# Optimization experiments

Measured on AMD Instinct MI355X. Metric: run time of the kernel, lower is better.

Reference implementation:

```python
import jax, jax.numpy as jnp
import numpy as np

H = 128; R = 8; VN = 100; VA = 64
N = 8192; B = 64; L = 48; E = 65536


def setup_inputs() -> dict:
    key = jax.random.key(0)
    ks = jax.random.split(key, 24)
    s = 0.05
    nodeTypes = jax.random.randint(ks[0], (N,), 0, VN)
    edge_index = jax.random.randint(ks[1], (2, E), 0, N)
    edge_attr = jax.random.randint(ks[2], (E,), 0, R)
    bs = jnp.repeat(jnp.arange(B), N // B)              # sorted node->graph map
    nodes_bs = jnp.full((B,), N // B, dtype=jnp.int32)  # nodes per graph
    len_seq = jax.random.randint(ks[3], (B,), 1, L + 1).at[0].set(L)  # max == L
    sequence_input = (jax.random.uniform(ks[4], (N, L)) < 0.05).astype(jnp.float32)
    action_input = jax.random.randint(ks[5], (B,), 0, VA)
    params = dict(
        emb_nodes=jax.random.normal(ks[6], (VN, H)) * s,
        emb_actions=jax.random.normal(ks[7], (VA, H)) * s,
        rgcn_rel=jax.random.normal(ks[8], (3, R, H, H)) * s,   # per-layer relation weights
        rgcn_root=jax.random.normal(ks[9], (3, H, H)) * s,
        rgcn_bias=jnp.zeros((3, H)),
        gru_w_ih=jax.random.normal(ks[10], (3 * H, H)) * s,
        gru_w_hh=jax.random.normal(ks[11], (3 * H, H)) * s,
        gru_b_ih=jnp.zeros((3 * H,)),
        gru_b_hh=jnp.zeros((3 * H,)),
        linA_w=jax.random.normal(ks[12], (H, H)) * s,
        linA_b=jnp.zeros((H,)),
        linAf_w=jax.random.normal(ks[13], (VA, H)) * s,
        linAf_b=jnp.zeros((VA,)),
        linN_w=jax.random.normal(ks[14], (H, 2 * H)) * s,
        linN_b=jnp.zeros((H,)),
        linNf_w=jax.random.normal(ks[15], (1, H)) * s,
        linNf_b=jnp.zeros((1,)),
    )
    return dict(nodeTypes=nodeTypes, edge_index=edge_index, edge_attr=edge_attr,
                bs=bs, nodes_bs=nodes_bs, len_seq=len_seq,
                sequence_input=sequence_input, action_input=action_input, **params)


def reference(nodeTypes, edge_index, edge_attr, bs, nodes_bs, len_seq,
              sequence_input, action_input,
              emb_nodes, emb_actions, rgcn_rel, rgcn_root, rgcn_bias,
              gru_w_ih, gru_w_hh, gru_b_ih, gru_b_hh,
              linA_w, linA_b, linAf_w, linAf_b,
              linN_w, linN_b, linNf_w, linNf_b):
    n = nodeTypes.shape[0]
    b = nodes_bs.shape[0]
    h = emb_nodes.shape[1]
    r = rgcn_rel.shape[1]
    l = sequence_input.shape[1]

    x = emb_nodes[nodeTypes]                               # [N,H]
    src, dst = edge_index[0], edge_index[1]
    seg = dst * r + edge_attr                              # per (target, relation) segment
    cnt = jax.ops.segment_sum(jnp.ones((src.shape[0],), x.dtype), seg, n * r)
    denom = jnp.maximum(cnt, 1.0).reshape(n, r, 1)
    for li in range(3):
        agg = jax.ops.segment_sum(x[src], seg, n * r).reshape(n, r, h) / denom
        x = jax.nn.relu(jnp.einsum('nrh,rho->no', agg, rgcn_rel[li])
                        + x @ rgcn_root[li] + rgcn_bias[li])

    # global mean pool -> graph embedding
    h_G = jax.ops.segment_sum(x, bs, b) / nodes_bs[:, None].astype(x.dtype)  # [B,H]
    action = jax.nn.relu(h_G @ linA_w.T + linA_b) @ linAf_w.T + linAf_b      # [B,VA]

    sos = emb_actions[action_input][:, None, :]            # [B,1,H]
    # sequence embeddings: sum over nodes in each graph of seq[i,t]*x[i]
    emb_seq = sequence_input[:, :, None] * x[:, None, :]   # [N,L,H]
    out = jax.ops.segment_sum(emb_seq, bs, b)              # [B,L,H]
    input_gru = jnp.concatenate([sos, out], axis=1)[:, :l] # packed GRU only sees first L steps

    # single-layer GRU, h0 = h_G (torch gate order r,z,n)
    xW = input_gru @ gru_w_ih.T + gru_b_ih                 # [B,L,3H]
    def step(hprev, xw):
        hW = hprev @ gru_w_hh.T + gru_b_hh
        xr, xz, xn = jnp.split(xw, 3, -1)
        hr, hz, hn = jnp.split(hW, 3, -1)
        rg = jax.nn.sigmoid(xr + hr)
        zg = jax.nn.sigmoid(xz + hz)
        ng = jnp.tanh(xn + rg * hn)
        hnew = (1.0 - zg) * ng + zg * hprev
        return hnew, hnew
    _, hs = jax.lax.scan(step, h_G, jnp.swapaxes(xW, 0, 1))
    seq_out = jnp.swapaxes(hs, 0, 1)                       # [B,L,H]
    mask = jnp.arange(l)[None, :] < len_seq[:, None]       # pad_packed zero-pads
    seq_out = seq_out * mask[:, :, None]

    out_gru = seq_out[bs]                                  # repeat_interleave -> [N,L,H]
    concats = jnp.concatenate(
        [out_gru, jnp.broadcast_to(x[:, None, :], (n, l, h))], axis=2)  # [N,L,2H]
    hid = jax.nn.relu(concats @ linN_w.T + linN_b)         # [N,L,H]
    logits = (hid @ linNf_w.T + linNf_b)[..., 0]           # [N,L]

    # scatter_softmax over nodes grouped by graph (dim 0)
    m = jax.lax.stop_gradient(jax.ops.segment_max(logits, bs, b))
    e = jnp.exp(logits - m[bs])
    ssum = jax.ops.segment_sum(e, bs, b)
    nodes_final = e / ssum[bs]
    return action, nodes_final
```

## Files before the change

### kernel.cpp

```cpp
#include <hip/hip_runtime.h>
#include <hip/hip_bf16.h>

#define H   128
#define RR  8
#define NN  8192
#define BB  64
#define LL  48
#define EE  65536
#define NPG 128
#define VA  64
#define NSEG (NN*RR)
#define GPB 16

typedef unsigned short u16;
typedef unsigned int   u32;

__device__ __forceinline__ float b2f(u16 u) {
    union { u32 i; float f; } v; v.i = ((u32)u) << 16; return v.f;
}
__device__ __forceinline__ u16 f2b(float f) {
    union { float f; u32 i; } v; v.f = f;
    u32 x = v.i;
    return (u16)((x + 0x7fffu + ((x >> 16) & 1u)) >> 16);
}
__device__ __forceinline__ float2 up2(u32 p) {
    union { u32 i; float f; } a, b;
    a.i = p << 16; b.i = p & 0xffff0000u;
    return make_float2(a.f, b.f);
}
__device__ __forceinline__ u32 pk2(float a, float b) {
    return ((u32)f2b(b) << 16) | (u32)f2b(a);
}
__device__ __forceinline__ float rcpf(float x) { return __builtin_amdgcn_rcpf(x); }
__device__ __forceinline__ u32 cvtpk(float lo, float hi) {
    u32 r;
    asm("v_cvt_pk_bf16_f32 %0, %1, %2" : "=v"(r) : "v"(lo), "v"(hi));
    return r;
}

#define K_LOG2E  1.4426950408889634f
#define K_2LOG2E 2.8853900817779268f

typedef __attribute__((ext_vector_type(8))) short bf16x8;
typedef __attribute__((ext_vector_type(4))) float f32x4;
typedef __attribute__((ext_vector_type(4))) unsigned short u16x4;

__global__ __launch_bounds__(256) void k_init(const int* __restrict__ nodeTypes,
                                              const float* __restrict__ emb_nodes,
                                              float* __restrict__ x0,
                                              int* __restrict__ fill) {
    int idx = blockIdx.x * 256 + threadIdx.x;
    if (idx < NSEG) fill[idx] = 0;
    if (idx < NN * H) {
        int n = idx >> 7, h = idx & (H - 1);
        x0[idx] = emb_nodes[(size_t)nodeTypes[n] * H + h];
    }
}

__global__ __launch_bounds__(256) void k_hist(const int* __restrict__ edge_index,
                                              const int* __restrict__ edge_attr,
                                              int* __restrict__ fill) {
    int e = blockIdx.x * 256 + threadIdx.x;
    if (e < EE) {
        int seg = edge_index[EE + e] * RR + edge_attr[e];
        atomicAdd(&fill[seg], 1);
    }
}

__global__ __launch_bounds__(256) void k_scan1(const int* __restrict__ fill,
                                               int* __restrict__ bsum) {
    __shared__ int red[4];
    int tid = threadIdx.x, lane = tid & 63, wv = tid >> 6;
    int v = fill[blockIdx.x * 256 + tid];
#pragma unroll
    for (int off = 32; off >= 1; off >>= 1) v += __shfl_down(v, off, 64);
    if (lane == 0) red[wv] = v;
    __syncthreads();
    if (tid == 0) bsum[blockIdx.x] = red[0] + red[1] + red[2] + red[3];
}

__global__ __launch_bounds__(256) void k_scan2(const int* __restrict__ bsum,
                                               int* __restrict__ boff,
                                               int* __restrict__ rowptr) {
    __shared__ int s[256];
    int tid = threadIdx.x;
    int v0 = bsum[tid];
    s[tid] = v0;
    __syncthreads();
    for (int off = 1; off < 256; off <<= 1) {
        int v = (tid >= off) ? s[tid - off] : 0;
        __syncthreads();
        s[tid] += v;
        __syncthreads();
    }
    boff[tid] = s[tid] - v0;
    if (tid == 255) rowptr[NSEG] = s[255];
}

__global__ __launch_bounds__(256) void k_scan3(const int* __restrict__ boff,
                                               int* __restrict__ fill,
                                               int* __restrict__ rowptr) {
    __shared__ int s[256];
    int tid = threadIdx.x;
    int g = blockIdx.x * 256 + tid;
    int c = fill[g];
    s[tid] = c;
    __syncthreads();
    for (int off = 1; off < 256; off <<= 1) {
        int v = (tid >= off) ? s[tid - off] : 0;
        __syncthreads();
        s[tid] += v;
        __syncthreads();
    }
    int r = boff[blockIdx.x] + s[tid] - c;
    rowptr[g] = r;
    fill[g] = r;
}

__global__ __launch_bounds__(256) void k_scatter(const int* __restrict__ edge_index,
                                                 const int* __restrict__ edge_attr,
                                                 int* __restrict__ fill,
                                                 int* __restrict__ colidx) {
    int e = blockIdx.x * 256 + threadIdx.x;
    if (e < EE) {
        int seg = edge_index[EE + e] * RR + edge_attr[e];
        int pos = atomicAdd(&fill[seg], 1);
        colidx[pos] = edge_index[e];
    }
}

__global__ __launch_bounds__(256) void k_wprep(const float* __restrict__ rel,
                                               const float* __restrict__ root,
                                               const float* __restrict__ w_ih,
                                               u16* __restrict__ WTt,
                                               u16* __restrict__ WTih,
                                               float* __restrict__ hGsum) {
    int idx = blockIdx.x * 256 + threadIdx.x;
    if (idx < 384 * H) WTih[idx] = f2b(w_ih[idx]);
    if (idx < BB * H) hGsum[idx] = 0.f;
    if (idx >= 3 * 147456) return;
    int li  = idx / 147456;
    int rem = idx - li * 147456;
    int tile = rem / 36864;
    int r2   = rem - tile * 36864;
    int ks   = r2 / 1024;
    int r3   = r2 - ks * 1024;
    int sub  = r3 >> 9;
    int r4   = r3 & 511;
    int lane = r4 >> 3, j = r4 & 7;
    int col = tile * 32 + sub * 16 + (lane & 15);
    int k   = ks * 32 + (lane >> 4) * 8 + j;
    float v;
    if (k < 1024) v = rel[(((size_t)li * RR + (k >> 7)) * H + (k & 127)) * H + col];
    else          v = root[((size_t)li * H + (k - 1024)) * H + col];
    WTt[idx] = f2b(v);
}

#define RGN 16
#define EPRE 512

__global__ __launch_bounds__(256) void k_rgcn(const float* __restrict__ xin,
                                              float* __restrict__ xout,
                                              const u16* __restrict__ WTt,
                                              const float* __restrict__ bias,
                                              const int* __restrict__ rowptr,
                                              const int* __restrict__ colidx,
                                              float* __restrict__ hGsum) {
    __shared__ u32 ab[RGN * 580];
    __shared__ int begs[RGN * RR + 1];
    __shared__ int eidx[EPRE];
    int tid = threadIdx.x, wv = tid >> 6, lane = tid & 63;
    int n0 = blockIdx.x * RGN, segbase = n0 * RR;

    if (tid <= RGN * RR) begs[tid] = rowptr[segbase + tid];
    __syncthreads();
    int E0 = begs[0], ne = begs[RGN * RR] - E0;
    for (int i = tid; i < ne && i < EPRE; i += 256) eidx[i] = colidx[E0 + i];
    __syncthreads();

    for (int s = wv; s < RGN * RR; s += 4) {
        int beg = begs[s], end = begs[s + 1];
        float a0 = 0.f, a1 = 0.f;
        for (int e = beg; e < end; ++e) {
            int off = e - E0;
            int src = (off < EPRE) ? eidx[off] : colidx[e];
            float2 v = ((const float2*)(xin + (size_t)src * H))[lane];
            a0 += v.x; a1 += v.y;
        }
        float inv = 1.f / fmaxf((float)(end - beg), 1.f);
        ab[(s >> 3) * 580 + ((s & 7) << 6) + lane] = pk2(a0 * inv, a1 * inv);
    }
    for (int i = wv; i < RGN; i += 4) {
        const float* xr = xin + (size_t)(n0 + i) * H + 2 * lane;
        ab[i * 580 + 512 + lane] = pk2(xr[0], xr[1]);
    }
    __syncthreads();

    int m = lane & 15, quad = lane >> 4;
    int colbase = wv * 32;
    const u32* aP = ab + m * 580 + quad * 4;
    const u32* bT = (const u32*)WTt + (size_t)wv * 36 * 512 + lane * 4;
    f32x4 acc0 = {0.f, 0.f, 0.f, 0.f}, acc1 = {0.f, 0.f, 0.f, 0.f};
    bf16x8 b0c = *(const bf16x8*)bT;
    bf16x8 b1c = *(const bf16x8*)(bT + 256);
    for (int ks = 0; ks < 36; ++ks) {
        bf16x8 b0n, b1n;
        if (ks < 35) {
            b0n = *(const bf16x8*)(bT + (ks + 1) * 512);
            b1n = *(const bf16x8*)(bT + (ks + 1) * 512 + 256);
        }
        bf16x8 a = *(const bf16x8*)(aP + ks * 16);
        acc0 = __builtin_amdgcn_mfma_f32_16x16x32_bf16(a, b0c, acc0, 0, 0, 0);
        acc1 = __builtin_amdgcn_mfma_f32_16x16x32_bf16(a, b1c, acc1, 0, 0, 0);
        b0c = b0n; b1c = b1n;
    }
    int c0 = colbase + m, c1 = c0 + 16;
    float bv0 = bias[c0], bv1 = bias[c1];
    float so0 = 0.f, so1 = 0.f;
#pragma unroll
    for (int rg = 0; rg < 4; ++rg) {
        int n = n0 + quad * 4 + rg;
        float o0 = fmaxf(acc0[rg] + bv0, 0.f);
        float o1 = fmaxf(acc1[rg] + bv1, 0.f);
        xout[(size_t)n * H + c0] = o0;
        xout[(size_t)n * H + c1] = o1;
        so0 += o0; so1 += o1;
    }
    if (hGsum) {
        so0 += __shfl_xor(so0, 16, 64);
        so0 += __shfl_xor(so0, 32, 64);
        so1 += __shfl_xor(so1, 16, 64);
        so1 += __shfl_xor(so1, 32, 64);
        if (quad == 0) {
            int g = n0 >> 7;
            atomicAdd(&hGsum[g * H + c0], so0);
            atomicAdd(&hGsum[g * H + c1], so1);
        }
    }
}

__global__ __launch_bounds__(128) void k_pool_act(const float* __restrict__ hGsum,
                                                  const int* __restrict__ nodes_bs,
                                                  const float* __restrict__ linA_w,
                                                  const float* __restrict__ linA_b,
                                                  const float* __restrict__ linAf_w,
                                                  const float* __restrict__ linAf_b,
                                                  float* __restrict__ hG,
                                                  float* __restrict__ out) {
    __shared__ float hgs[H], t1[H];
    int b = blockIdx.x, h = threadIdx.x;
    float hg = hGsum[(size_t)b * H + h] / (float)nodes_bs[b];
    hG[(size_t)b * H + h] = hg;
    hgs[h] = hg;
    __syncthreads();
    float acc = linA_b[h];
    const float* wr = linA_w + (size_t)h * H;
    for (int k = 0; k < H; ++k) acc += wr[k] * hgs[k];
    t1[h] = fmaxf(acc, 0.f);
    __syncthreads();
    if (h < VA) {
        float a = linAf_b[h];
        const float* w2 = linAf_w + (size_t)h * H;
        for (int k = 0; k < H; ++k) a += w2[k] * t1[k];
        out[(size_t)b * VA + h] = a;
    }
}

__global__ __launch_bounds__(256) void k_seqpool(const float* __restrict__ xf,
                                                 const float* __restrict__ seq,
                                                 const float* __restrict__ emb_actions,
                                                 const int* __restrict__ action_input,
                                                 float* __restrict__ igG) {
    __shared__ float xg[64][H];
    __shared__ u16 lists[LL][64];
    __shared__ int cnts[LL];
    int b = blockIdx.x, tid = threadIdx.x;
    int col = tid & 127, tg = tid >> 7;
    float acc[24];
#pragma unroll
    for (int m = 0; m < 24; ++m) acc[m] = 0.f;

    for (int chunk = 0; chunk < 2; ++chunk) {
        int i0 = b * NPG + chunk * 64;
        __syncthreads();
        if (tid < LL) cnts[tid] = 0;
        __syncthreads();
        for (int idx = tid; idx < 64 * H / 4; idx += 256)
            ((float4*)&xg[0][0])[idx] = ((const float4*)(xf + (size_t)i0 * H))[idx];
        for (int idx = tid; idx < 64 * LL; idx += 256) {
            int i = idx / LL, t = idx - i * LL;
            if (seq[(size_t)(i0 + i) * LL + t] != 0.f) {
                int p = atomicAdd(&cnts[t], 1);
                lists[t][p] = (u16)i;
            }
        }
        __syncthreads();
        for (int m = 0; m < 24; ++m) {
            int t = tg + 2 * m;
            int c = cnts[t];
            float a = acc[m];
            for (int p = 0; p < c; ++p) a += xg[lists[t][p]][col];
            acc[m] = a;
        }
    }
    if (tid < H)
        igG[((size_t)b * LL) * H + tid] = emb_actions[(size_t)action_input[b] * H + tid];
#pragma unroll
    for (int m = 0; m < 24; ++m) {
        int t = tg + 2 * m;
        if (t < LL - 1)
            igG[((size_t)b * LL + t + 1) * H + col] = acc[m];
    }
}

__global__ __launch_bounds__(256) void k_xw(const float* __restrict__ igG,
                                            const u16* __restrict__ WTih,
                                            const float* __restrict__ b_ih,
                                            const float* __restrict__ b_hh,
                                            u16* __restrict__ xwG) {
    __shared__ u32 ab[16 * 68];
    int tid = threadIdx.x, wv = tid >> 6, lane = tid & 63;
    int n0 = blockIdx.x * 16;
    for (int s = tid; s < 16 * 64; s += 256) {
        int row = s >> 6, kp = s & 63;
        float2 v = *(const float2*)(igG + (size_t)(n0 + row) * H + 2 * kp);
        ab[row * 68 + kp] = pk2(v.x, v.y);
    }
    __syncthreads();
    int m = lane & 15, quad = lane >> 4;
    const u32* aP = ab + m * 68 + quad * 4;
    f32x4 acc[6];
#pragma unroll
    for (int i = 0; i < 6; ++i) acc[i] = (f32x4){0.f, 0.f, 0.f, 0.f};
#pragma unroll
    for (int ks = 0; ks < 4; ++ks) {
        bf16x8 a = *(const bf16x8*)(aP + ks * 16);
#pragma unroll
        for (int tc = 0; tc < 6; ++tc) {
            int colr = wv * 96 + tc * 16 + m;
            bf16x8 bfr = *(const bf16x8*)((const u32*)WTih + (size_t)colr * 64 + quad * 4 + ks * 16);
            acc[tc] = __builtin_amdgcn_mfma_f32_16x16x32_bf16(a, bfr, acc[tc], 0, 0, 0);
        }
    }
#pragma unroll
    for (int tc = 0; tc < 6; ++tc) {
        int c = wv * 96 + tc * 16 + m;
        float bv = b_ih[c] + ((c < 256) ? b_hh[c] : 0.f);
        float sc = (c < 256) ? K_LOG2E : K_2LOG2E;
        int R = c & 127, gate = c >> 7;
#pragma unroll
        for (int rg = 0; rg < 4; ++rg) {
            int r = n0 + quad * 4 + rg;
            int bb = r / 48, tt = r - bb * 48;
            size_t o = (((((size_t)(bb >> 4) * LL + tt) * 8 + (R >> 4)) * 3 + gate) * 256)
                     + (((R >> 2) & 3) << 6) + ((bb & 15) << 2) + (R & 3);
            xwG[o] = f2b((acc[tc][rg] + bv) * sc);
        }
    }
}

__global__ __launch_bounds__(512) void k_gruM(const u16* __restrict__ xw2,
                                              const float* __restrict__ hG,
                                              const float* __restrict__ w_hh,
                                              const float* __restrict__ b_hh,
                                              const int* __restrict__ len_seq,
                                              float* __restrict__ soutG) {
    __shared__ __align__(16) u16 hA[2][2][2048];
    int tid = threadIdx.x;
    int lane = tid & 63, wv = tid >> 6;
    int mi = lane & 15, quad = lane >> 4;
    int gblk = blockIdx.x;
    int g_abs = gblk * GPB + mi;
    int R0 = 16 * wv + 4 * quad;

    int eW = (((wv >> 1) * 64) + (mi + 16 * ((2 * wv + (quad >> 1)) & 3))) * 8
             + 4 * (quad & 1);

    bf16x8 wfr[3][4];
#pragma unroll
    for (int gate = 0; gate < 3; ++gate) {
        int T = wv + 8 * gate;
        float sc = (gate == 2) ? K_2LOG2E : K_LOG2E;
#pragma unroll
        for (int ks = 0; ks < 4; ++ks) {
            const float* wp = w_hh + (size_t)(16 * T + mi) * H + quad * 8 + ks * 32;
            float4 f0 = *(const float4*)wp;
            float4 f1 = *(const float4*)(wp + 4);
            bf16x8 v;
            v[0] = (short)f2b(f0.x * sc); v[1] = (short)f2b(f0.y * sc);
            v[2] = (short)f2b(f0.z * sc); v[3] = (short)f2b(f0.w * sc);
            v[4] = (short)f2b(f1.x * sc); v[5] = (short)f2b(f1.y * sc);
            v[6] = (short)f2b(f1.z * sc); v[7] = (short)f2b(f1.w * sc);
            wfr[gate][ks] = v;
        }
    }
    float4 bn = *(const float4*)(b_hh + 256 + R0);
    float4 h0 = *(const float4*)(hG + (size_t)g_abs * H + R0);
    int ls = len_seq[g_abs];

    float hp[4]  = {h0.x, h0.y, h0.z, h0.w};
    float bnn[4] = {bn.x * K_2LOG2E, bn.y * K_2LOG2E, bn.z * K_2LOG2E, bn.w * K_2LOG2E};

    auto storeh = [&](int buf, const float* hv) {
        u32 w0 = cvtpk(hv[0], hv[1]);
        u32 w1 = cvtpk(hv[2], hv[3]);
        float2 e0 = up2(w0), e1 = up2(w1);
        u32 l0 = cvtpk(hv[0] - e0.x, hv[1] - e0.y);
        u32 l1 = cvtpk(hv[2] - e1.x, hv[3] - e1.y);
        *(uint2*)&hA[buf][0][eW] = make_uint2(w0, w1);
        *(uint2*)&hA[buf][1][eW] = make_uint2(l0, l1);
    };
    auto loadxw = [&](int t, u16x4* d) {
        const u16* p = xw2 + ((((size_t)gblk * LL + t) * 8 + wv) * 3) * 256
                     + (quad << 6) + (mi << 2);
        d[0] = *(const u16x4*)(p);
        d[1] = *(const u16x4*)(p + 256);
        d[2] = *(const u16x4*)(p + 512);
    };

    auto step = [&](int t, const u16x4* x, int buf) {
        f32x4 acc[3];
        acc[0] = (f32x4){0.f, 0.f, 0.f, 0.f};
        acc[1] = (f32x4){0.f, 0.f, 0.f, 0.f};
        acc[2] = (f32x4){bnn[0], bnn[1], bnn[2], bnn[3]};
#pragma unroll
        for (int ks = 0; ks < 4; ++ks) {
            const int e = (ks * 64 + lane) * 8;
            bf16x8 bh = *(const bf16x8*)&hA[buf][0][e];
            bf16x8 bl = *(const bf16x8*)&hA[buf][1][e];
#pragma unroll
            for (int gate = 0; gate < 3; ++gate) {
                acc[gate] = __builtin_amdgcn_mfma_f32_16x16x32_bf16(wfr[gate][ks], bh, acc[gate], 0, 0, 0);
                acc[gate] = __builtin_amdgcn_mfma_f32_16x16x32_bf16(wfr[gate][ks], bl, acc[gate], 0, 0, 0);
            }
        }
        float hv[4];
        float4 so;
#pragma unroll
        for (int r = 0; r < 4; ++r) {
            float xr = b2f(x[0][r]);
            float xz = b2f(x[1][r]);
            float xn = b2f(x[2][r]);
            float rg = rcpf(1.f + __builtin_amdgcn_exp2f(-(xr + acc[0][r])));
            float zg = rcpf(1.f + __builtin_amdgcn_exp2f(-(xz + acc[1][r])));
            float u  = xn + rg * acc[2][r];
            float ng = 1.f - 2.f * rcpf(__builtin_amdgcn_exp2f(u) + 1.f);
            float hn = ng + zg * (hp[r] - ng);
            hp[r] = hn;
            hv[r] = hn;
            ((float*)&so)[r] = (t < ls) ? hn : 0.f;
        }
        *(float4*)(soutG + ((size_t)g_abs * LL + t) * H + R0) = so;
        storeh(buf ^ 1, hv);
    };

    u16x4 xa[3], xb[3];
    loadxw(0, xa);
    loadxw(1, xb);
    storeh(0, hp);
    asm volatile("s_waitcnt lgkmcnt(0)\n\ts_barrier" ::: "memory");

    for (int t = 0; t < LL; t += 2) {
        step(t, xa, 0);
        if (t + 2 < LL) loadxw(t + 2, xa);
        asm volatile("s_waitcnt lgkmcnt(0)\n\ts_barrier" ::: "memory");
        step(t + 1, xb, 1);
        if (t + 3 < LL) loadxw(t + 3, xb);
        asm volatile("s_waitcnt lgkmcnt(0)\n\ts_barrier" ::: "memory");
    }
}

__global__ __launch_bounds__(256) void k_a2(const float* __restrict__ soutG,
                                            const float* __restrict__ linN_w,
                                            float* __restrict__ A2) {
    __shared__ float wb[32][130];
    __shared__ float xl[16][H];
    int tid = threadIdx.x;
    int n0 = blockIdx.x * 16;
    for (int idx = tid; idx < 16 * H; idx += 256)
        xl[idx >> 7][idx & 127] = soutG[(size_t)n0 * H + idx];
    int col = tid & 127, g = tid >> 7;
    float acc[8] = {0.f, 0.f, 0.f, 0.f, 0.f, 0.f, 0.f, 0.f};
    for (int c = 0; c < 4; ++c) {
        int k0 = c * 32;
        __syncthreads();
        for (int idx = tid; idx < 32 * H; idx += 256) {
            int r = idx >> 5, kk = idx & 31;
            wb[kk][r] = linN_w[(size_t)r * (2 * H) + k0 + kk];
        }
        __syncthreads();
#pragma unroll
        for (int kk = 0; kk < 32; ++kk) {
            float w = wb[kk][col];
#pragma unroll
            for (int j = 0; j < 8; ++j) acc[j] += xl[g * 8 + j][k0 + kk] * w;
        }
    }
#pragma unroll
    for (int j = 0; j < 8; ++j)
        A2[(size_t)(n0 + g * 8 + j) * H + col] = acc[j];
}

__global__ __launch_bounds__(256) void k_bx(const float* __restrict__ xf,
                                            const float* __restrict__ linN_w,
                                            const float* __restrict__ linN_b,
                                            u16* __restrict__ BxU) {
    __shared__ float wb[32][130];
    __shared__ float xl[16][H];
    int tid = threadIdx.x;
    int n0 = blockIdx.x * 16;
    for (int idx = tid; idx < 16 * H; idx += 256)
        xl[idx >> 7][idx & 127] = xf[(size_t)n0 * H + idx];
    int col = tid & 127, g = tid >> 7;
    float bv = linN_b[col];
    float acc[8] = {bv, bv, bv, bv, bv, bv, bv, bv};
    for (int c = 0; c < 4; ++c) {
        int k0 = c * 32;
        __syncthreads();
        for (int idx = tid; idx < 32 * H; idx += 256) {
            int r = idx >> 5, kk = idx & 31;
            wb[kk][r] = linN_w[(size_t)r * (2 * H) + H + k0 + kk];
        }
        __syncthreads();
#pragma unroll
        for (int kk = 0; kk < 32; ++kk) {
            float w = wb[kk][col];
#pragma unroll
            for (int j = 0; j < 8; ++j) acc[j] += xl[g * 8 + j][k0 + kk] * w;
        }
    }
#pragma unroll
    for (int j = 0; j < 8; ++j)
        BxU[(size_t)(n0 + g * 8 + j) * H + col] = f2b(acc[j]);
}

__global__ __launch_bounds__(256) void k_logits(const float* __restrict__ A2,
                                                const u16* __restrict__ BxU,
                                                const float* __restrict__ linNf_w,
                                                float* __restrict__ logits) {
    __shared__ float a2s[LL][130];
    __shared__ float bxs[16][130];
    __shared__ float w2s[H];
    int tid = threadIdx.x;
    int g = blockIdx.x >> 3, tile = blockIdx.x & 7;
    int n0g = g * NPG + tile * 16;

    for (int i2 = tid; i2 < LL * 64; i2 += 256) {
        int r = i2 >> 6, c2 = i2 & 63;
        *(float2*)&a2s[r][2 * c2] = *(const float2*)(A2 + ((size_t)g * LL + r) * H + 2 * c2);
    }
    for (int iu = tid; iu < 16 * 64; iu += 256) {
        int r = iu >> 6, c = iu & 63;
        float2 v = up2(((const u32*)BxU)[(size_t)(n0g + r) * 64 + c]);
        *(float2*)&bxs[r][2 * c] = v;
    }
    if (tid < H) w2s[tid] = linNf_w[tid];
    __syncthreads();

    int n = tid & 15, tt = tid >> 4;
#pragma unroll
    for (int pass = 0; pass < 3; ++pass) {
        int t = tt + 16 * pass;
        float acc = 0.f;
#pragma unroll
        for (int kp = 0; kp < 64; ++kp) {
            float2 a2 = *(const float2*)&a2s[t][2 * kp];
            float2 bx = *(const float2*)&bxs[n][2 * kp];
            float2 w  = *(const float2*)&w2s[2 * kp];
            acc += w.x * fmaxf(a2.x + bx.x, 0.f) + w.y * fmaxf(a2.y + bx.y, 0.f);
        }
        logits[(size_t)(n0g + n) * LL + t] = acc;
    }
}

__global__ __launch_bounds__(256) void k_softmax(const float* __restrict__ logits,
                                                 float* __restrict__ out) {
    __shared__ float lg[NPG][LL + 1];
    __shared__ float pm[4][LL], ps[4][LL];
    __shared__ float mv[LL], inv[LL];
    int b = blockIdx.x, tid = threadIdx.x;
    int n0 = b * NPG;
    for (int idx = tid; idx < NPG * LL; idx += 256) {
        int n = idx / LL, t = idx - n * LL;
        lg[n][t] = logits[(size_t)n0 * LL + idx];
    }
    __syncthreads();
    int t = tid & 63, seg = tid >> 6;
    if (t < LL) {
        float m = -1e30f;
        int nb = seg * 32;
        for (int n = nb; n < nb + 32; ++n) m = fmaxf(m, lg[n][t]);
        pm[seg][t] = m;
    }
    __syncthreads();
    if (tid < LL)
        mv[tid] = fmaxf(fmaxf(pm[0][tid], pm[1][tid]), fmaxf(pm[2][tid], pm[3][tid]));
    __syncthreads();
    if (t < LL) {
        float m = mv[t], s = 0.f;
        int nb = seg * 32;
        for (int n = nb; n < nb + 32; ++n) {
            float e = __expf(lg[n][t] - m);
            lg[n][t] = e;
            s += e;
        }
        ps[seg][t] = s;
    }
    __syncthreads();
    if (tid < LL)
        inv[tid] = 1.f / (ps[0][tid] + ps[1][tid] + ps[2][tid] + ps[3][tid]);
    __syncthreads();
    for (int idx = tid; idx < NPG * LL; idx += 256) {
        int n = idx / LL, tc = idx - n * LL;
        out[(size_t)BB * VA + (size_t)n0 * LL + idx] = lg[n][tc] * inv[tc];
    }
}

extern "C" void kernel_launch(void* const* d_in, const int* in_sizes, int n_in,
                              void* d_out, int out_size, void* d_ws, size_t ws_size,
                              hipStream_t stream) {
    (void)in_sizes; (void)n_in; (void)out_size; (void)ws_size;
    const int*   nodeTypes    = (const int*)d_in[0];
    const int*   edge_index   = (const int*)d_in[1];
    const int*   edge_attr    = (const int*)d_in[2];
    const int*   nodes_bs     = (const int*)d_in[4];
    const int*   len_seq      = (const int*)d_in[5];
    const float* seq_in       = (const float*)d_in[6];
    const int*   action_input = (const int*)d_in[7];
    const float* emb_nodes    = (const float*)d_in[8];
    const float* emb_actions  = (const float*)d_in[9];
    const float* rgcn_rel     = (const float*)d_in[10];
    const float* rgcn_root    = (const float*)d_in[11];
    const float* rgcn_bias    = (const float*)d_in[12];
    const float* gru_w_ih     = (const float*)d_in[13];
    const float* gru_w_hh     = (const float*)d_in[14];
    const float* gru_b_ih     = (const float*)d_in[15];
    const float* gru_b_hh     = (const float*)d_in[16];
    const float* linA_w       = (const float*)d_in[17];
    const float* linA_b       = (const float*)d_in[18];
    const float* linAf_w      = (const float*)d_in[19];
    const float* linAf_b      = (const float*)d_in[20];
    const float* linN_w       = (const float*)d_in[21];
    const float* linN_b       = (const float*)d_in[22];
    const float* linNf_w      = (const float*)d_in[23];

    char* w = (char*)d_ws;
    float* x0      = (float*)(w + 0);
    u16*   xwG     = (u16*)  (w + 0);
    float* logitsW = (float*)(w + 0);
    float* soutG   = (float*)(w + 2359296);
    float* x1      = (float*)(w + 4194304);
    float* igG     = (float*)(w + 8388608);
    float* A2      = (float*)(w + 8388608);
    u16*   BxU     = (u16*)  (w + 9961472);
    int*   bsum    = (int*)  (w + 9961472);
    int*   boff    = (int*)  (w + 9962496);
    float* hGsum   = (float*)(w + 9969664);
    int*   rowptr  = (int*)  (w + 11567104);
    int*   fill    = (int*)  (w + 11829760);
    u16*   WTih    = (u16*)  (w + 11829760);
    float* hG      = (float*)(w + 12058624);
    int*   colidx  = (int*)  (w + 12091904);
    u16*   WT      = (u16*)  (w + 12616192);

    float* out_f = (float*)d_out;

    k_init<<<dim3(4096), dim3(256), 0, stream>>>(nodeTypes, emb_nodes, x0, fill);
    k_hist<<<dim3(256), dim3(256), 0, stream>>>(edge_index, edge_attr, fill);
    k_scan1<<<dim3(256), dim3(256), 0, stream>>>(fill, bsum);
    k_scan2<<<dim3(1), dim3(256), 0, stream>>>(bsum, boff, rowptr);
    k_scan3<<<dim3(256), dim3(256), 0, stream>>>(boff, fill, rowptr);
    k_scatter<<<dim3(256), dim3(256), 0, stream>>>(edge_index, edge_attr, fill, colidx);
    k_wprep<<<dim3(1728), dim3(256), 0, stream>>>(rgcn_rel, rgcn_root, gru_w_ih,
                                                  WT, WTih, hGsum);

    const int rg_grid = NN / RGN;
    k_rgcn<<<dim3(rg_grid), dim3(256), 0, stream>>>(x0, x1,
        WT + 0 * 147456, rgcn_bias + 0 * H, rowptr, colidx, nullptr);
    k_rgcn<<<dim3(rg_grid), dim3(256), 0, stream>>>(x1, x0,
        WT + 1 * 147456, rgcn_bias + 1 * H, rowptr, colidx, nullptr);
    k_rgcn<<<dim3(rg_grid), dim3(256), 0, stream>>>(x0, x1,
        WT + 2 * 147456, rgcn_bias + 2 * H, rowptr, colidx, hGsum);

    k_pool_act<<<dim3(BB), dim3(128), 0, stream>>>(hGsum, nodes_bs, linA_w, linA_b,
                                                   linAf_w, linAf_b, hG, out_f);
    k_seqpool<<<dim3(BB), dim3(256), 0, stream>>>(x1, seq_in, emb_actions, action_input, igG);
    k_xw<<<dim3(BB * LL / 16), dim3(256), 0, stream>>>(igG, WTih, gru_b_ih, gru_b_hh, xwG);
    k_gruM<<<dim3(BB / GPB), dim3(512), 0, stream>>>(xwG, hG, gru_w_hh, gru_b_hh,
                                                     len_seq, soutG);
    k_a2<<<dim3(BB * LL / 16), dim3(256), 0, stream>>>(soutG, linN_w, A2);
    k_bx<<<dim3(NN / 16), dim3(256), 0, stream>>>(x1, linN_w, linN_b, BxU);
    k_logits<<<dim3(BB * 8), dim3(256), 0, stream>>>(A2, BxU, linNf_w, logitsW);
    k_softmax<<<dim3(BB), dim3(256), 0, stream>>>(logitsW, out_f);
}
```

Before: 364.3 us.

## Fuse node projection into GRU launch and widen RGCN blocks to eight waves

The RGCN kernel now runs 512 threads per block, so each wave computes one 16-column MFMA tile instead of two and edge gathering is split across eight waves. The independent node-side linear projection (BxU) is folded into the serial GRU launch as extra blocks. Those blocks run on otherwise idle CUs while the 4 GRU blocks step through the sequence, removing one launch and its serialized time. The cost is more threads per block, possibly lower occupancy, in the RGCN kernel, and a shared-memory union sized to the larger of the two roles.

```diff
diff --git a/kernel.cpp b/kernel.cpp
--- a/kernel.cpp
+++ b/kernel.cpp
@@ -159,7 +159,7 @@
 #define RGN 16
 #define EPRE 512
 
-__global__ __launch_bounds__(256) void k_rgcn(const float* __restrict__ xin,
+__global__ __launch_bounds__(512) void k_rgcn(const float* __restrict__ xin,
                                               float* __restrict__ xout,
                                               const u16* __restrict__ WTt,
                                               const float* __restrict__ bias,
@@ -175,10 +175,10 @@
     if (tid <= RGN * RR) begs[tid] = rowptr[segbase + tid];
     __syncthreads();
     int E0 = begs[0], ne = begs[RGN * RR] - E0;
-    for (int i = tid; i < ne && i < EPRE; i += 256) eidx[i] = colidx[E0 + i];
-    __syncthreads();
-
-    for (int s = wv; s < RGN * RR; s += 4) {
+    for (int i = tid; i < ne && i < EPRE; i += 512) eidx[i] = colidx[E0 + i];
+    __syncthreads();
+
+    for (int s = wv; s < RGN * RR; s += 8) {
         int beg = begs[s], end = begs[s + 1];
         float a0 = 0.f, a1 = 0.f;
         for (int e = beg; e < end; ++e) {
@@ -190,51 +190,40 @@
         float inv = 1.f / fmaxf((float)(end - beg), 1.f);
         ab[(s >> 3) * 580 + ((s & 7) << 6) + lane] = pk2(a0 * inv, a1 * inv);
     }
-    for (int i = wv; i < RGN; i += 4) {
+    for (int i = wv; i < RGN; i += 8) {
         const float* xr = xin + (size_t)(n0 + i) * H + 2 * lane;
         ab[i * 580 + 512 + lane] = pk2(xr[0], xr[1]);
     }
     __syncthreads();
 
     int m = lane & 15, quad = lane >> 4;
-    int colbase = wv * 32;
     const u32* aP = ab + m * 580 + quad * 4;
-    const u32* bT = (const u32*)WTt + (size_t)wv * 36 * 512 + lane * 4;
-    f32x4 acc0 = {0.f, 0.f, 0.f, 0.f}, acc1 = {0.f, 0.f, 0.f, 0.f};
+    const u32* bT = (const u32*)WTt + (size_t)(wv >> 1) * 36 * 512 + (wv & 1) * 256 + lane * 4;
+    f32x4 acc0 = {0.f, 0.f, 0.f, 0.f};
     bf16x8 b0c = *(const bf16x8*)bT;
-    bf16x8 b1c = *(const bf16x8*)(bT + 256);
     for (int ks = 0; ks < 36; ++ks) {
-        bf16x8 b0n, b1n;
-        if (ks < 35) {
-            b0n = *(const bf16x8*)(bT + (ks + 1) * 512);
-            b1n = *(const bf16x8*)(bT + (ks + 1) * 512 + 256);
-        }
+        bf16x8 b0n;
+        if (ks < 35) b0n = *(const bf16x8*)(bT + (ks + 1) * 512);
         bf16x8 a = *(const bf16x8*)(aP + ks * 16);
         acc0 = __builtin_amdgcn_mfma_f32_16x16x32_bf16(a, b0c, acc0, 0, 0, 0);
-        acc1 = __builtin_amdgcn_mfma_f32_16x16x32_bf16(a, b1c, acc1, 0, 0, 0);
-        b0c = b0n; b1c = b1n;
-    }
-    int c0 = colbase + m, c1 = c0 + 16;
-    float bv0 = bias[c0], bv1 = bias[c1];
-    float so0 = 0.f, so1 = 0.f;
+        b0c = b0n;
+    }
+    int c0 = wv * 16 + m;
+    float bv0 = bias[c0];
+    float so0 = 0.f;
 #pragma unroll
     for (int rg = 0; rg < 4; ++rg) {
         int n = n0 + quad * 4 + rg;
         float o0 = fmaxf(acc0[rg] + bv0, 0.f);
-        float o1 = fmaxf(acc1[rg] + bv1, 0.f);
         xout[(size_t)n * H + c0] = o0;
-        xout[(size_t)n * H + c1] = o1;
-        so0 += o0; so1 += o1;
+        so0 += o0;
     }
     if (hGsum) {
         so0 += __shfl_xor(so0, 16, 64);
         so0 += __shfl_xor(so0, 32, 64);
-        so1 += __shfl_xor(so1, 16, 64);
-        so1 += __shfl_xor(so1, 32, 64);
         if (quad == 0) {
             int g = n0 >> 7;
             atomicAdd(&hGsum[g * H + c0], so0);
-            atomicAdd(&hGsum[g * H + c1], so1);
         }
     }
 }
@@ -359,14 +348,55 @@
     }
 }
 
-__global__ __launch_bounds__(512) void k_gruM(const u16* __restrict__ xw2,
-                                              const float* __restrict__ hG,
-                                              const float* __restrict__ w_hh,
-                                              const float* __restrict__ b_hh,
-                                              const int* __restrict__ len_seq,
-                                              float* __restrict__ soutG) {
-    __shared__ __align__(16) u16 hA[2][2][2048];
+#define GRU_BLKS 4
+#define BX_BLKS  (NN / 32)
+#define SMEM_BYTES 33024
+
+__global__ __launch_bounds__(512) void k_gru_bx(const u16* __restrict__ xw2,
+                                                const float* __restrict__ hG,
+                                                const float* __restrict__ w_hh,
+                                                const float* __restrict__ b_hh,
+                                                const int* __restrict__ len_seq,
+                                                float* __restrict__ soutG,
+                                                const float* __restrict__ xf,
+                                                const float* __restrict__ linN_w,
+                                                const float* __restrict__ linN_b,
+                                                u16* __restrict__ BxU) {
+    __shared__ __align__(16) char smem[SMEM_BYTES];
     int tid = threadIdx.x;
+
+    if (blockIdx.x >= GRU_BLKS) {
+        float* xl = (float*)smem;
+        float* wb = (float*)(smem + 16384);
+        int bid = blockIdx.x - GRU_BLKS;
+        int n0 = bid * 32;
+        for (int idx = tid; idx < 32 * H; idx += 512)
+            xl[idx] = xf[(size_t)n0 * H + idx];
+        int col = tid & 127, g = tid >> 7;
+        float bv = linN_b[col];
+        float acc[8] = {bv, bv, bv, bv, bv, bv, bv, bv};
+        for (int c = 0; c < 4; ++c) {
+            int k0 = c * 32;
+            __syncthreads();
+            for (int idx = tid; idx < 32 * H; idx += 512) {
+                int r = idx >> 5, kk = idx & 31;
+                wb[kk * 130 + r] = linN_w[(size_t)r * (2 * H) + H + k0 + kk];
+            }
+            __syncthreads();
+#pragma unroll
+            for (int kk = 0; kk < 32; ++kk) {
+                float w = wb[kk * 130 + col];
+#pragma unroll
+                for (int j = 0; j < 8; ++j) acc[j] += xl[(g * 8 + j) * H + k0 + kk] * w;
+            }
+        }
+#pragma unroll
+        for (int j = 0; j < 8; ++j)
+            BxU[(size_t)(n0 + g * 8 + j) * H + col] = f2b(acc[j]);
+        return;
+    }
+
+    u16* hA = (u16*)smem;
     int lane = tid & 63, wv = tid >> 6;
     int mi = lane & 15, quad = lane >> 4;
     int gblk = blockIdx.x;
@@ -407,8 +437,8 @@
         float2 e0 = up2(w0), e1 = up2(w1);
         u32 l0 = cvtpk(hv[0] - e0.x, hv[1] - e0.y);
         u32 l1 = cvtpk(hv[2] - e1.x, hv[3] - e1.y);
-        *(uint2*)&hA[buf][0][eW] = make_uint2(w0, w1);
-        *(uint2*)&hA[buf][1][eW] = make_uint2(l0, l1);
+        *(uint2*)&hA[buf * 4096 + eW]        = make_uint2(w0, w1);
+        *(uint2*)&hA[buf * 4096 + 2048 + eW] = make_uint2(l0, l1);
     };
     auto loadxw = [&](int t, u16x4* d) {
         const u16* p = xw2 + ((((size_t)gblk * LL + t) * 8 + wv) * 3) * 256
@@ -426,8 +456,8 @@
 #pragma unroll
         for (int ks = 0; ks < 4; ++ks) {
             const int e = (ks * 64 + lane) * 8;
-            bf16x8 bh = *(const bf16x8*)&hA[buf][0][e];
-            bf16x8 bl = *(const bf16x8*)&hA[buf][1][e];
+            bf16x8 bh = *(const bf16x8*)&hA[buf * 4096 + e];
+            bf16x8 bl = *(const bf16x8*)&hA[buf * 4096 + 2048 + e];
 #pragma unroll
             for (int gate = 0; gate < 3; ++gate) {
                 acc[gate] = __builtin_amdgcn_mfma_f32_16x16x32_bf16(wfr[gate][ks], bh, acc[gate], 0, 0, 0);
@@ -499,39 +529,6 @@
 #pragma unroll
     for (int j = 0; j < 8; ++j)
         A2[(size_t)(n0 + g * 8 + j) * H + col] = acc[j];
-}
-
-__global__ __launch_bounds__(256) void k_bx(const float* __restrict__ xf,
-                                            const float* __restrict__ linN_w,
-                                            const float* __restrict__ linN_b,
-                                            u16* __restrict__ BxU) {
-    __shared__ float wb[32][130];
-    __shared__ float xl[16][H];
-    int tid = threadIdx.x;
-    int n0 = blockIdx.x * 16;
-    for (int idx = tid; idx < 16 * H; idx += 256)
-        xl[idx >> 7][idx & 127] = xf[(size_t)n0 * H + idx];
-    int col = tid & 127, g = tid >> 7;
-    float bv = linN_b[col];
-    float acc[8] = {bv, bv, bv, bv, bv, bv, bv, bv};
-    for (int c = 0; c < 4; ++c) {
-        int k0 = c * 32;
-        __syncthreads();
-        for (int idx = tid; idx < 32 * H; idx += 256) {
-            int r = idx >> 5, kk = idx & 31;
-            wb[kk][r] = linN_w[(size_t)r * (2 * H) + H + k0 + kk];
-        }
-        __syncthreads();
-#pragma unroll
-        for (int kk = 0; kk < 32; ++kk) {
-            float w = wb[kk][col];
-#pragma unroll
-            for (int j = 0; j < 8; ++j) acc[j] += xl[g * 8 + j][k0 + kk] * w;
-        }
-    }
-#pragma unroll
-    for (int j = 0; j < 8; ++j)
-        BxU[(size_t)(n0 + g * 8 + j) * H + col] = f2b(acc[j]);
 }
 
 __global__ __launch_bounds__(256) void k_logits(const float* __restrict__ A2,
@@ -675,21 +672,20 @@
                                                   WT, WTih, hGsum);
 
     const int rg_grid = NN / RGN;
-    k_rgcn<<<dim3(rg_grid), dim3(256), 0, stream>>>(x0, x1,
+    k_rgcn<<<dim3(rg_grid), dim3(512), 0, stream>>>(x0, x1,
         WT + 0 * 147456, rgcn_bias + 0 * H, rowptr, colidx, nullptr);
-    k_rgcn<<<dim3(rg_grid), dim3(256), 0, stream>>>(x1, x0,
+    k_rgcn<<<dim3(rg_grid), dim3(512), 0, stream>>>(x1, x0,
         WT + 1 * 147456, rgcn_bias + 1 * H, rowptr, colidx, nullptr);
-    k_rgcn<<<dim3(rg_grid), dim3(256), 0, stream>>>(x0, x1,
+    k_rgcn<<<dim3(rg_grid), dim3(512), 0, stream>>>(x0, x1,
         WT + 2 * 147456, rgcn_bias + 2 * H, rowptr, colidx, hGsum);
 
     k_pool_act<<<dim3(BB), dim3(128), 0, stream>>>(hGsum, nodes_bs, linA_w, linA_b,
                                                    linAf_w, linAf_b, hG, out_f);
     k_seqpool<<<dim3(BB), dim3(256), 0, stream>>>(x1, seq_in, emb_actions, action_input, igG);
     k_xw<<<dim3(BB * LL / 16), dim3(256), 0, stream>>>(igG, WTih, gru_b_ih, gru_b_hh, xwG);
-    k_gruM<<<dim3(BB / GPB), dim3(512), 0, stream>>>(xwG, hG, gru_w_hh, gru_b_hh,
-                                                     len_seq, soutG);
+    k_gru_bx<<<dim3(GRU_BLKS + BX_BLKS), dim3(512), 0, stream>>>(xwG, hG, gru_w_hh,
+        gru_b_hh, len_seq, soutG, x1, linN_w, linN_b, BxU);
     k_a2<<<dim3(BB * LL / 16), dim3(256), 0, stream>>>(soutG, linN_w, A2);
-    k_bx<<<dim3(NN / 16), dim3(256), 0, stream>>>(x1, linN_w, linN_b, BxU);
     k_logits<<<dim3(BB * 8), dim3(256), 0, stream>>>(A2, BxU, linNf_w, logitsW);
     k_softmax<<<dim3(BB), dim3(256), 0, stream>>>(logitsW, out_f);
 }
```

Result: faster. 321.6 us (-11.7%).
